# Optimization experiments

Hardware: AMD Instinct MI355X
Metric: run time of the kernel (lower is better)

## Reference

```python
import jax, jax.numpy as jnp
import numpy as np

B, A, N_OBS, HX, N_ACT = 8192, 32, 128, 64, 16

def setup_inputs() -> dict:
    key = jax.random.key(0)
    ks = jax.random.split(key, 12)
    s = lambda *shape: 0.05 * jax.random.normal(ks[setup_inputs.i], shape, dtype=jnp.float32)
    out = {}
    setup_inputs.i = 0
    def nxt(*shape):
        setup_inputs.i += 1
        return 0.05 * jax.random.normal(ks[setup_inputs.i], shape, dtype=jnp.float32)
    out['obs'] = jax.random.normal(ks[0], (B, A, N_OBS), dtype=jnp.float32)
    out['W1'] = nxt(A, N_OBS, 128); out['b1'] = nxt(A, 128)
    out['W2'] = nxt(A, 128, HX);   out['b2'] = nxt(A, HX)
    out['Wg'] = nxt(A, HX, 2);     out['bg'] = nxt(A, 2)
    out['Wc'] = nxt(A, 2 * HX, HX); out['bc'] = nxt(A, HX)
    out['Wd'] = nxt(A, HX, N_ACT); out['bd'] = nxt(A, N_ACT)
    out['comm_mask'] = jax.random.randint(jax.random.fold_in(key, 99), (A, A), 0, 2, dtype=jnp.int32)
    return out

def reference(obs, W1, b1, W2, b2, Wg, bg, Wc, bc, Wd, bd, comm_mask):
    # encode: per-agent 2-layer MLP, batched over agents via einsum
    x = jax.nn.relu(jnp.einsum('ban,anh->bah', obs, W1) + b1)      # [B,A,128]
    h = jax.nn.relu(jnp.einsum('bah,ahk->bak', x, W2) + b2)        # [B,A,HX]
    # gate: Linear->ReLU->Softmax (computed as in original; only used via the
    # host-side RNG in the torch code, externalized here as comm_mask)
    gates = jax.nn.softmax(jax.nn.relu(jnp.einsum('bak,akg->bag', h, Wg) + bg), axis=-1)
    # communication: for agent i, mean of hidden states of communicating j != i
    mask = comm_mask.astype(h.dtype) * (1.0 - jnp.eye(A, dtype=h.dtype))  # [A_i, A_j]
    total = jnp.einsum('ij,bjk->bik', mask, h)                      # [B,A,HX]
    count = mask.sum(axis=1)                                        # [A]
    comm = total / jnp.maximum(count, 1.0)[None, :, None]           # count==0 -> zeros
    comm_in = jnp.concatenate([h, comm], axis=-1)                   # [B,A,2*HX]
    h2 = jnp.tanh(jnp.einsum('bac,ack->bak', comm_in, Wc) + bc)     # [B,A,HX]
    q = jnp.einsum('bak,akn->ban', h2, Wd) + bd                     # [B,A,N_ACT]
    return q
```

## Files before the change

kernel.cpp:

```cpp
#include <hip/hip_runtime.h>


#define NB   8192
#define NA   32
#define NOBS 128
#define NH1  128
#define HXX  64
#define NACT 16

typedef _Float16 half8 __attribute__((ext_vector_type(8)));
typedef _Float16 half4 __attribute__((ext_vector_type(4)));
typedef float    floatx4 __attribute__((ext_vector_type(4)));

#define MFMA16(af, bf, c) __builtin_amdgcn_mfma_f32_16x16x32_f16((af), (bf), (c), 0, 0, 0)
#define H8(x) __builtin_bit_cast(half8, (x))

#define HWS_OFF 0
#define W1P_OFF (NB * NA * HXX)
#define W1P_CNT (NA * 8 * 4 * 512)
#define W2P_OFF (W1P_OFF + W1P_CNT)
#define W2P_CNT (NA * 4 * 4 * 512)
#define WCP_OFF (W2P_OFF + W2P_CNT)
#define WCP_CNT (NA * 4 * 4 * 512)
#define WDP_OFF (WCP_OFF + WCP_CNT)
#define WDP_CNT (NA * 1 * 2 * 512)
#define MN_OFF  (WDP_OFF + WDP_CNT)
#define PACK_TOTAL (W1P_CNT + W2P_CNT + WCP_CNT + WDP_CNT)

#define HSTR 2056
#define DEC_LDS (16 * HSTR * 2)

#define ENC_TILES 8
#define ENC_WROWS 128
#define ENC_BROWS 1024
#define ENC_SLAB  16384
#define ENC_W2LDS (8 * ENC_SLAB)
#define ENC_LDS   (ENC_W2LDS + 16384)

using gas1p = const __attribute__((address_space(1))) void*;
using las3p = __attribute__((address_space(3))) void*;

__device__ __forceinline__ float fast_tanh(float x) {
    x = fminf(fmaxf(x, -10.f), 10.f);
    float e2 = __expf(2.f * x);
    return (e2 - 1.f) / (e2 + 1.f);
}

extern "C" __global__ void pack_kernel(const float* __restrict__ W1,
                                       const float* __restrict__ W2,
                                       const float* __restrict__ Wc,
                                       const float* __restrict__ Wd,
                                       const int*   __restrict__ cmask,
                                       _Float16* __restrict__ ws)
{
    int e = blockIdx.x * 256 + threadIdx.x;
    if (e >= PACK_TOTAL + NA * NA) return;
    if (e >= PACK_TOTAL) {
        int r = e - PACK_TOTAL, i = r >> 5, j = r & 31;
        int c = 0;
        for (int jj = 0; jj < NA; ++jj) c += (jj != i && cmask[i * NA + jj]) ? 1 : 0;
        float v = 0.f;
        if (j != i && cmask[i * NA + j]) v = 1.0f / (float)(c > 1 ? c : 1);
        ((float*)(ws + MN_OFF))[r] = v;
        return;
    }
    const float* src; _Float16* dst; int K, N, NT, NS, r;
    if (e < W1P_CNT) {
        src = W1; dst = ws + W1P_OFF; K = 128; N = 128; NT = 8; NS = 4; r = e;
    } else if (e < W1P_CNT + W2P_CNT) {
        src = W2; dst = ws + W2P_OFF; K = 128; N = 64; NT = 4; NS = 4; r = e - W1P_CNT;
    } else if (e < W1P_CNT + W2P_CNT + WCP_CNT) {
        src = Wc; dst = ws + WCP_OFF; K = 128; N = 64; NT = 4; NS = 4; r = e - W1P_CNT - W2P_CNT;
    } else {
        src = Wd; dst = ws + WDP_OFF; K = 64; N = 16; NT = 1; NS = 2; r = e - W1P_CNT - W2P_CNT - WCP_CNT;
    }
    int j = r & 7, l = (r >> 3) & 63;
    int rest = r >> 9;
    int s  = rest % NS; rest /= NS;
    int nt = rest % NT; rest /= NT;
    int a  = rest;
    int k = s * 32 + (l >> 4) * 8 + j;
    int n = nt * 16 + (l & 15);
    dst[r] = (_Float16)src[((size_t)a * K + k) * N + n];
}

extern "C" __global__ __launch_bounds__(512, 2)
void enc_kernel(const float* __restrict__ obs,
                const float* __restrict__ b1,
                const float* __restrict__ b2,
                const _Float16* __restrict__ W1p,
                const _Float16* __restrict__ W2p,
                _Float16* __restrict__ hws)
{
    extern __shared__ char smem[];

    const int tid  = threadIdx.x;
    const int a    = blockIdx.y;
    const int w    = tid >> 6, l = tid & 63;
    const int lm   = l & 15, lq = l >> 4;
    const int hrow = l >> 5;
    const int cch  = l & 31;
    char* SBA = smem + w * ENC_SLAB;
    char* SBB = SBA + 8192;
    _Float16* W2L = (_Float16*)(smem + ENC_W2LDS);

    {
        const uint4* s = (const uint4*)(W2p + (size_t)a * (4 * 4 * 512));
        uint4* d = (uint4*)W2L;
        d[tid]       = s[tid];
        d[tid + 512] = s[tid + 512];
    }

    const int rowb = blockIdx.x * ENC_BROWS + w * ENC_WROWS;
    const char* ob = (const char*)obs + (size_t)rowb * (NA * NOBS * 4) + (size_t)a * (NOBS * 4);

    floatx4 w1r[8][4];
    #pragma unroll
    for (int nt = 0; nt < 8; ++nt)
        #pragma unroll
        for (int s = 0; s < 4; ++s)
            w1r[nt][s] = *(const floatx4*)&W1p[(((a * 8 + nt) * 4 + s) * 512) + l * 8];
    float b1v[8], b2v[4];
    #pragma unroll
    for (int nt = 0; nt < 8; ++nt) b1v[nt] = b1[a * NH1 + nt * 16 + lm];
    #pragma unroll
    for (int nt = 0; nt < 4; ++nt) b2v[nt] = b2[a * HXX + nt * 16 + lm];

    #pragma unroll
    for (int nt = 0; nt < 8; ++nt)
        #pragma unroll
        for (int s = 0; s < 4; ++s) asm volatile("" :: "v"(w1r[nt][s]));
    #pragma unroll
    for (int nt = 0; nt < 8; ++nt) asm volatile("" :: "v"(b1v[nt]));
    #pragma unroll
    for (int nt = 0; nt < 4; ++nt) asm volatile("" :: "v"(b2v[nt]));

    int dmaoff[8];
    #pragma unroll
    for (int i = 0; i < 8; ++i) {
        const int r = 2 * i + hrow;
        dmaoff[i] = r * (NA * NOBS * 4) + ((cch ^ (r & 7)) << 4);
    }

    auto issue = [&](int t, char* dst) {
        const char* bt = ob + (size_t)t * (16 * NA * NOBS * 4);
        #pragma unroll
        for (int i = 0; i < 8; ++i)
            __builtin_amdgcn_global_load_lds((gas1p)(bt + dmaoff[i]),
                                             (las3p)(dst + i * 1024), 16, 0, 0);
    };

    issue(0, SBA);
    __syncthreads();

    for (int t = 0; t < ENC_TILES; ++t) {
        char* SBp = (t & 1) ? SBB : SBA;
        char* SBn = (t & 1) ? SBA : SBB;

        if (t < ENC_TILES - 1) {
            asm volatile("s_waitcnt lgkmcnt(0)" ::: "memory");
            issue(t + 1, SBn);
            if (t == 0) asm volatile("s_waitcnt vmcnt(8)" ::: "memory");
            else        asm volatile("s_waitcnt vmcnt(10)" ::: "memory");
        } else {
            asm volatile("s_waitcnt vmcnt(2)" ::: "memory");
        }
        __builtin_amdgcn_sched_barrier(0);

        _Float16* X = (_Float16*)SBp;
        const int rx = lm & 7;

        floatx4 acc1[8];
        #pragma unroll
        for (int nt = 0; nt < 8; ++nt) acc1[nt] = (floatx4){0.f, 0.f, 0.f, 0.f};
        #pragma unroll
        for (int s = 0; s < 4; ++s) {
            const int c0 = s * 8 + lq * 2;
            floatx4 f0 = *(const floatx4*)(SBp + lm * 512 + (((c0    ) ^ rx) << 4));
            floatx4 f1 = *(const floatx4*)(SBp + lm * 512 + (((c0 + 1) ^ rx) << 4));
            half8 af;
            af[0] = (_Float16)f0[0]; af[1] = (_Float16)f0[1];
            af[2] = (_Float16)f0[2]; af[3] = (_Float16)f0[3];
            af[4] = (_Float16)f1[0]; af[5] = (_Float16)f1[1];
            af[6] = (_Float16)f1[2]; af[7] = (_Float16)f1[3];
            #pragma unroll
            for (int nt = 0; nt < 8; ++nt)
                acc1[nt] = MFMA16(af, H8(w1r[nt][s]), acc1[nt]);
        }
        #pragma unroll
        for (int nt = 0; nt < 8; ++nt)
            #pragma unroll
            for (int v = 0; v < 4; ++v) {
                float xv = fmaxf(acc1[nt][v] + b1v[nt], 0.f);
                X[(lq * 4 + v) * 136 + nt * 16 + lm] = (_Float16)xv;
            }

        floatx4 acc2[4];
        #pragma unroll
        for (int nt = 0; nt < 4; ++nt) acc2[nt] = (floatx4){0.f, 0.f, 0.f, 0.f};
        #pragma unroll
        for (int s = 0; s < 4; ++s) {
            half8 af2 = *(const half8*)&X[lm * 136 + s * 32 + lq * 8];
            #pragma unroll
            for (int nt = 0; nt < 4; ++nt) {
                half8 bf = *(const half8*)&W2L[(nt * 4 + s) * 512 + l * 8];
                acc2[nt] = MFMA16(af2, bf, acc2[nt]);
            }
        }
        #pragma unroll
        for (int nt = 0; nt < 4; ++nt)
            #pragma unroll
            for (int v = 0; v < 4; ++v) {
                float hv = fmaxf(acc2[nt][v] + b2v[nt], 0.f);
                X[(lq * 4 + v) * 136 + nt * 16 + lm] = (_Float16)hv;
            }

        {
            const int rr = l >> 2, cc = l & 3;
            _Float16* hb = hws + ((size_t)(rowb + t * 16 + rr) * NA + a) * HXX;
            #pragma unroll
            for (int q2 = 0; q2 < 2; ++q2) {
                const int chunk = cc + 4 * q2;
                half8 hv8 = *(const half8*)&X[rr * 136 + chunk * 8];
                *(half8*)&hb[chunk * 8] = hv8;
            }
        }
    }
}

extern "C" __global__ __launch_bounds__(512)
void dec_kernel(const _Float16* __restrict__ hws,
                const float* __restrict__ MnG,
                const float* __restrict__ bc,
                const float* __restrict__ bd,
                const _Float16* __restrict__ Wcp,
                const _Float16* __restrict__ Wdp,
                float* __restrict__ out)
{
    extern __shared__ char smem[];
    _Float16* H = (_Float16*)smem;

    const int t  = threadIdx.x;
    const int b0 = blockIdx.x * 16;

    {
        const uint4* src = (const uint4*)(hws + (size_t)b0 * NA * HXX);
        #pragma unroll
        for (int it = 0; it < 8; ++it) {
            int idx = it * 512 + t;
            int row = idx >> 8, rem = idx & 255;
            *(uint4*)&H[row * HSTR + rem * 8] = src[idx];
        }
    }
    __syncthreads();

    const int w = t >> 6, l = t & 63, lm = l & 15, lq = l >> 4;

    half8 hacc[4][2];
    #pragma unroll
    for (int g = 0; g < 4; ++g)
        #pragma unroll
        for (int sb = 0; sb < 2; ++sb)
            #pragma unroll
            for (int q = 0; q < 8; ++q) hacc[g][sb][q] = (_Float16)0.f;

    #pragma unroll 4
    for (int j = 0; j < NA; ++j) {
        half8 v0 = *(const half8*)&H[lm * HSTR + j * 64 + lq * 8];
        half8 v1 = *(const half8*)&H[lm * HSTR + j * 64 + 32 + lq * 8];
        #pragma unroll
        for (int g = 0; g < 4; ++g) {
            int ag = __builtin_amdgcn_readfirstlane(w * 4 + g);
            _Float16 mh = (_Float16)MnG[ag * NA + j];
            hacc[g][0] += v0 * mh;
            hacc[g][1] += v1 * mh;
        }
    }
    __syncthreads();

    half4 h2r[4][4];
    #pragma unroll
    for (int nt = 0; nt < 4; ++nt) {
        floatx4 acc[4];
        #pragma unroll
        for (int g = 0; g < 4; ++g) acc[g] = (floatx4){0.f, 0.f, 0.f, 0.f};
        #pragma unroll
        for (int s = 0; s < 4; ++s) {
            #pragma unroll
            for (int g = 0; g < 4; ++g) {
                int ag = w * 4 + g;
                half8 af = (s < 2)
                    ? *(const half8*)&H[lm * HSTR + ag * 64 + s * 32 + lq * 8]
                    : hacc[g][s - 2];
                half8 bf = *(const half8*)&Wcp[(((ag * 4 + nt) * 4 + s) * 512) + l * 8];
                acc[g] = MFMA16(af, bf, acc[g]);
            }
        }
        #pragma unroll
        for (int g = 0; g < 4; ++g) {
            int ag = w * 4 + g;
            float bcv = bc[ag * HXX + nt * 16 + lm];
            #pragma unroll
            for (int v = 0; v < 4; ++v)
                h2r[g][nt][v] = (_Float16)fast_tanh(acc[g][v] + bcv);
        }
    }

    #pragma unroll
    for (int g = 0; g < 4; ++g) {
        int ag = w * 4 + g;
        #pragma unroll
        for (int nt = 0; nt < 4; ++nt)
            #pragma unroll
            for (int v = 0; v < 4; ++v)
                H[(lq * 4 + v) * HSTR + ag * 64 + nt * 16 + lm] = h2r[g][nt][v];
    }

    floatx4 acc3[4];
    #pragma unroll
    for (int g = 0; g < 4; ++g) acc3[g] = (floatx4){0.f, 0.f, 0.f, 0.f};
    #pragma unroll
    for (int s = 0; s < 2; ++s) {
        #pragma unroll
        for (int g = 0; g < 4; ++g) {
            int ag = w * 4 + g;
            half8 af = *(const half8*)&H[lm * HSTR + ag * 64 + s * 32 + lq * 8];
            half8 bf = *(const half8*)&Wdp[((ag * 2 + s) * 512) + l * 8];
            acc3[g] = MFMA16(af, bf, acc3[g]);
        }
    }

    #pragma unroll
    for (int g = 0; g < 4; ++g) {
        int ag = w * 4 + g;
        float bdv = bd[ag * NACT + lm];
        #pragma unroll
        for (int v = 0; v < 4; ++v) {
            int row = lq * 4 + v;
            out[((size_t)(b0 + row) * NA + ag) * NACT + lm] = acc3[g][v] + bdv;
        }
    }
}

extern "C" void kernel_launch(void* const* d_in, const int* in_sizes, int n_in,
                              void* d_out, int out_size, void* d_ws, size_t ws_size,
                              hipStream_t stream)
{
    const float* obs = (const float*)d_in[0];
    const float* W1  = (const float*)d_in[1];
    const float* b1  = (const float*)d_in[2];
    const float* W2  = (const float*)d_in[3];
    const float* b2  = (const float*)d_in[4];
    const float* Wc  = (const float*)d_in[7];
    const float* bc  = (const float*)d_in[8];
    const float* Wd  = (const float*)d_in[9];
    const float* bd  = (const float*)d_in[10];
    const int*   cm  = (const int*)d_in[11];

    float*    outp = (float*)d_out;
    _Float16* ws   = (_Float16*)d_ws;

    _Float16* hws = ws + HWS_OFF;
    _Float16* W1p = ws + W1P_OFF;
    _Float16* W2p = ws + W2P_OFF;
    _Float16* Wcp = ws + WCP_OFF;
    _Float16* Wdp = ws + WDP_OFF;
    const float* MnG = (const float*)(ws + MN_OFF);

    hipLaunchKernelGGL(pack_kernel, dim3((PACK_TOTAL + NA * NA + 255) / 256),
                       dim3(256), 0, stream, W1, W2, Wc, Wd, cm, ws);

    (void)hipFuncSetAttribute((const void*)enc_kernel,
                              hipFuncAttributeMaxDynamicSharedMemorySize, ENC_LDS);
    hipLaunchKernelGGL(enc_kernel, dim3(NB / ENC_BROWS, NA), dim3(512), ENC_LDS,
                       stream, obs, b1, b2, W1p, W2p, hws);

    (void)hipFuncSetAttribute((const void*)dec_kernel,
                              hipFuncAttributeMaxDynamicSharedMemorySize, DEC_LDS);
    hipLaunchKernelGGL(dec_kernel, dim3(NB / 16), dim3(512), DEC_LDS, stream,
                       hws, MnG, bc, bd, Wcp, Wdp, outp);
}
```

Baseline: 272.5 us.

## Deepen encoder obs prefetch to four stages and tile pack kernel per wave

The encoder moves from 8 waves with double-buffered obs tiles to 4 waves per block, each handling 256 rows through a 4-deep ring of global-to-LDS loads with hand-tuned vmcnt waits. The aim is more bytes in flight per wave to hide HBM latency while LDS use stays about the same. Occupancy is now one 256-thread block per launch bound, so fewer waves are resident to hide latency. The pack kernel is also rewritten so each wave stages one 16x32 fragment in LDS and writes half8 vectors, replacing scattered scalar fp16 stores.

After: 275.5 us. No clear change (+1.1%).

```diff
diff --git a/kernel.cpp b/kernel.cpp
--- a/kernel.cpp
+++ b/kernel.cpp
@@ -25,17 +25,20 @@
 #define WDP_OFF (WCP_OFF + WCP_CNT)
 #define WDP_CNT (NA * 1 * 2 * 512)
 #define MN_OFF  (WDP_OFF + WDP_CNT)
-#define PACK_TOTAL (W1P_CNT + W2P_CNT + WCP_CNT + WDP_CNT)
 
 #define HSTR 2056
 #define DEC_LDS (16 * HSTR * 2)
 
-#define ENC_TILES 8
-#define ENC_WROWS 128
+#define ENC_TILES 16
+#define ENC_WROWS 256
 #define ENC_BROWS 1024
-#define ENC_SLAB  16384
-#define ENC_W2LDS (8 * ENC_SLAB)
+#define ENC_DEPTH 4
+#define ENC_SLAB  (ENC_DEPTH * 8192)
+#define ENC_W2LDS (4 * ENC_SLAB)
 #define ENC_LDS   (ENC_W2LDS + 16384)
+
+#define PK_FRAG_BLOCKS 528
+#define PK_BLOCKS      (PK_FRAG_BLOCKS + 4)
 
 using gas1p = const __attribute__((address_space(1))) void*;
 using las3p = __attribute__((address_space(3))) void*;
@@ -46,17 +49,21 @@
     return (e2 - 1.f) / (e2 + 1.f);
 }
 
-extern "C" __global__ void pack_kernel(const float* __restrict__ W1,
-                                       const float* __restrict__ W2,
-                                       const float* __restrict__ Wc,
-                                       const float* __restrict__ Wd,
-                                       const int*   __restrict__ cmask,
-                                       _Float16* __restrict__ ws)
+extern "C" __global__ __launch_bounds__(256)
+void pack_kernel(const float* __restrict__ W1,
+                 const float* __restrict__ W2,
+                 const float* __restrict__ Wc,
+                 const float* __restrict__ Wd,
+                 const int*   __restrict__ cmask,
+                 _Float16* __restrict__ ws)
 {
-    int e = blockIdx.x * 256 + threadIdx.x;
-    if (e >= PACK_TOTAL + NA * NA) return;
-    if (e >= PACK_TOTAL) {
-        int r = e - PACK_TOTAL, i = r >> 5, j = r & 31;
+    __shared__ float stg[4][512];
+    const int bid = blockIdx.x, tid = threadIdx.x;
+
+    if (bid >= PK_FRAG_BLOCKS) {
+        int r = (bid - PK_FRAG_BLOCKS) * 256 + tid;
+        if (r >= NA * NA) return;
+        int i = r >> 5, j = r & 31;
         int c = 0;
         for (int jj = 0; jj < NA; ++jj) c += (jj != i && cmask[i * NA + jj]) ? 1 : 0;
         float v = 0.f;
@@ -64,27 +71,61 @@
         ((float*)(ws + MN_OFF))[r] = v;
         return;
     }
-    const float* src; _Float16* dst; int K, N, NT, NS, r;
-    if (e < W1P_CNT) {
-        src = W1; dst = ws + W1P_OFF; K = 128; N = 128; NT = 8; NS = 4; r = e;
-    } else if (e < W1P_CNT + W2P_CNT) {
-        src = W2; dst = ws + W2P_OFF; K = 128; N = 64; NT = 4; NS = 4; r = e - W1P_CNT;
-    } else if (e < W1P_CNT + W2P_CNT + WCP_CNT) {
-        src = Wc; dst = ws + WCP_OFF; K = 128; N = 64; NT = 4; NS = 4; r = e - W1P_CNT - W2P_CNT;
+
+    const int w = tid >> 6, l = tid & 63;
+    const int W = bid * 4 + w;
+
+    const float* src; _Float16* dst; int K, N;
+    int a, nt, s;
+    if (W < 1024) {
+        int q = W; a = q >> 5; nt = (q >> 2) & 7; s = q & 3;
+        src = W1; N = 128; K = 128;
+        dst = ws + W1P_OFF + ((a * 8 + nt) * 4 + s) * 512;
+    } else if (W < 1536) {
+        int q = W - 1024; a = q >> 4; nt = (q >> 2) & 3; s = q & 3;
+        src = W2; N = 64; K = 128;
+        dst = ws + W2P_OFF + ((a * 4 + nt) * 4 + s) * 512;
+    } else if (W < 2048) {
+        int q = W - 1536; a = q >> 4; nt = (q >> 2) & 3; s = q & 3;
+        src = Wc; N = 64; K = 128;
+        dst = ws + WCP_OFF + ((a * 4 + nt) * 4 + s) * 512;
     } else {
-        src = Wd; dst = ws + WDP_OFF; K = 64; N = 16; NT = 1; NS = 2; r = e - W1P_CNT - W2P_CNT - WCP_CNT;
-    }
-    int j = r & 7, l = (r >> 3) & 63;
-    int rest = r >> 9;
-    int s  = rest % NS; rest /= NS;
-    int nt = rest % NT; rest /= NT;
-    int a  = rest;
-    int k = s * 32 + (l >> 4) * 8 + j;
-    int n = nt * 16 + (l & 15);
-    dst[r] = (_Float16)src[((size_t)a * K + k) * N + n];
-}
-
-extern "C" __global__ __launch_bounds__(512, 2)
+        int q = W - 2048; a = q >> 1; nt = 0; s = q & 1;
+        src = Wd; N = 16; K = 64;
+        dst = ws + WDP_OFF + (a * 2 + s) * 512;
+    }
+
+    const float* base = src + (size_t)a * K * N + (size_t)(s * 32) * N + nt * 16;
+    float* S = stg[w];
+
+    #pragma unroll
+    for (int p = 0; p < 8; ++p) {
+        int e = p * 64 + l, kk = e >> 4, nn = e & 15;
+        S[kk * 16 + nn] = base[(size_t)kk * N + nn];
+    }
+    asm volatile("s_waitcnt lgkmcnt(0)" ::: "memory");
+    __builtin_amdgcn_sched_barrier(0);
+
+    half8 hv;
+    #pragma unroll
+    for (int j = 0; j < 8; ++j)
+        hv[j] = (_Float16)S[((l >> 4) * 8 + j) * 16 + (l & 15)];
+    *(half8*)&dst[l * 8] = hv;
+}
+
+__device__ __forceinline__ void enc_wait_vm(int t) {
+    switch (t) {
+    case 0:  asm volatile("s_waitcnt vmcnt(24)" ::: "memory"); break;
+    case 1:  asm volatile("s_waitcnt vmcnt(26)" ::: "memory"); break;
+    case 2:  asm volatile("s_waitcnt vmcnt(28)" ::: "memory"); break;
+    case 13: asm volatile("s_waitcnt vmcnt(22)" ::: "memory"); break;
+    case 14: asm volatile("s_waitcnt vmcnt(14)" ::: "memory"); break;
+    case 15: asm volatile("s_waitcnt vmcnt(6)"  ::: "memory"); break;
+    default: asm volatile("s_waitcnt vmcnt(30)" ::: "memory"); break;
+    }
+}
+
+extern "C" __global__ __launch_bounds__(256, 1)
 void enc_kernel(const float* __restrict__ obs,
                 const float* __restrict__ b1,
                 const float* __restrict__ b2,
@@ -100,15 +141,14 @@
     const int lm   = l & 15, lq = l >> 4;
     const int hrow = l >> 5;
     const int cch  = l & 31;
-    char* SBA = smem + w * ENC_SLAB;
-    char* SBB = SBA + 8192;
+    char* SB = smem + w * ENC_SLAB;
     _Float16* W2L = (_Float16*)(smem + ENC_W2LDS);
 
     {
         const uint4* s = (const uint4*)(W2p + (size_t)a * (4 * 4 * 512));
         uint4* d = (uint4*)W2L;
-        d[tid]       = s[tid];
-        d[tid + 512] = s[tid + 512];
+        #pragma unroll
+        for (int q = 0; q < 4; ++q) d[tid + 256 * q] = s[tid + 256 * q];
     }
 
     const int rowb = blockIdx.x * ENC_BROWS + w * ENC_WROWS;
@@ -142,29 +182,25 @@
         dmaoff[i] = r * (NA * NOBS * 4) + ((cch ^ (r & 7)) << 4);
     }
 
-    auto issue = [&](int t, char* dst) {
+    auto issue = [&](int t) {
         const char* bt = ob + (size_t)t * (16 * NA * NOBS * 4);
+        char* dstb = SB + (t & 3) * 8192;
         #pragma unroll
         for (int i = 0; i < 8; ++i)
             __builtin_amdgcn_global_load_lds((gas1p)(bt + dmaoff[i]),
-                                             (las3p)(dst + i * 1024), 16, 0, 0);
+                                             (las3p)(dstb + i * 1024), 16, 0, 0);
     };
 
-    issue(0, SBA);
     __syncthreads();
 
+    issue(0); issue(1); issue(2);
+
     for (int t = 0; t < ENC_TILES; ++t) {
-        char* SBp = (t & 1) ? SBB : SBA;
-        char* SBn = (t & 1) ? SBA : SBB;
-
-        if (t < ENC_TILES - 1) {
-            asm volatile("s_waitcnt lgkmcnt(0)" ::: "memory");
-            issue(t + 1, SBn);
-            if (t == 0) asm volatile("s_waitcnt vmcnt(8)" ::: "memory");
-            else        asm volatile("s_waitcnt vmcnt(10)" ::: "memory");
-        } else {
-            asm volatile("s_waitcnt vmcnt(2)" ::: "memory");
-        }
+        char* SBp = SB + (t & 3) * 8192;
+
+        asm volatile("s_waitcnt lgkmcnt(0)" ::: "memory");
+        if (t <= ENC_TILES - 4) issue(t + 3);
+        enc_wait_vm(t);
         __builtin_amdgcn_sched_barrier(0);
 
         _Float16* X = (_Float16*)SBp;
@@ -367,12 +403,12 @@
     _Float16* Wdp = ws + WDP_OFF;
     const float* MnG = (const float*)(ws + MN_OFF);
 
-    hipLaunchKernelGGL(pack_kernel, dim3((PACK_TOTAL + NA * NA + 255) / 256),
-                       dim3(256), 0, stream, W1, W2, Wc, Wd, cm, ws);
+    hipLaunchKernelGGL(pack_kernel, dim3(PK_BLOCKS), dim3(256), 0, stream,
+                       W1, W2, Wc, Wd, cm, ws);
 
     (void)hipFuncSetAttribute((const void*)enc_kernel,
                               hipFuncAttributeMaxDynamicSharedMemorySize, ENC_LDS);
-    hipLaunchKernelGGL(enc_kernel, dim3(NB / ENC_BROWS, NA), dim3(512), ENC_LDS,
+    hipLaunchKernelGGL(enc_kernel, dim3(NB / ENC_BROWS, NA), dim3(256), ENC_LDS,
                        stream, obs, b1, b2, W1p, W2p, hws);
 
     (void)hipFuncSetAttribute((const void*)dec_kernel,
```
